# Kernel tuning notes

Hardware: AMD Instinct MI355X
Metric: run time of the kernel (lower is better)

## Reference

```python
import jax, jax.numpy as jnp
import numpy as np

K = 3   # kernel_size
D = 1   # dilation
G = 8   # groups
BN_EPS = 1e-5


def setup_inputs() -> dict:
    key = jax.random.key(0)
    ks = jax.random.split(key, 8)
    N, C, H, W = 8, 64, 256, 256
    k2 = K * K
    x = jax.random.normal(ks[0], (N, C, H, W), jnp.float32)
    conv_w = jax.random.normal(ks[1], (G * k2, C), jnp.float32) * (2.0 / C) ** 0.5
    bn_gamma = jnp.ones((G * k2,), jnp.float32)
    bn_beta = jnp.zeros((G * k2,), jnp.float32)
    bn_mean = jax.random.normal(ks[2], (G * k2,), jnp.float32) * 0.01
    bn_var = jax.random.uniform(ks[3], (G * k2,), jnp.float32, 0.5, 1.5)
    lamb_l = jax.random.normal(ks[4], (C,), jnp.float32) * 0.1
    lamb_h = jax.random.normal(ks[5], (C,), jnp.float32) * 0.1
    inside_all = jax.random.normal(ks[6], (C, 1, 1), jnp.float32) * 0.1
    return {"x": x, "conv_w": conv_w, "bn_gamma": bn_gamma, "bn_beta": bn_beta,
            "bn_mean": bn_mean, "bn_var": bn_var, "lamb_l": lamb_l,
            "lamb_h": lamb_h, "inside_all": inside_all}


def reference(x, conv_w, bn_gamma, bn_beta, bn_mean, bn_var, lamb_l, lamb_h, inside_all):
    N, C, H, W = x.shape
    k2 = K * K
    # ap: adaptive avg pool to (1,1) -> (N, C)
    pooled = x.mean(axis=(2, 3))
    # 1x1 conv on a 1x1 map == matmul; then eval-mode BatchNorm
    lf = pooled @ conv_w.T                                   # (N, G*k2)
    lf = (lf - bn_mean) * (bn_gamma / jnp.sqrt(bn_var + BN_EPS)) + bn_beta
    lf = jnp.tanh(lf).reshape(N, G, 1, k2, 1)                # (N, G, 1, k2, 1)
    # im2col/unfold with reflection padding; ordering matches torch (C, kh, kw)
    p = D * (K - 1) // 2
    xp = jnp.pad(x, ((0, 0), (0, 0), (p, p), (p, p)), mode="reflect")
    patches = jnp.stack(
        [xp[:, :, i * D:i * D + H, j * D:j * D + W] for i in range(K) for j in range(K)],
        axis=2,
    )                                                        # (N, C, k2, H, W)
    xu = patches.reshape(N, G, C // G, k2, H * W)
    low_part = jnp.sum(xu * lf, axis=3).reshape(N, C, H, W)  # per-pixel dynamic filter
    # DSA: gap pools to (1,1)
    gap = x.mean(axis=(2, 3), keepdims=True)                 # (N, C, 1, 1)
    out_low = (low_part * (inside_all + 1.0) - inside_all * gap) * lamb_l[None, :, None, None]
    out_high = x * (lamb_h[None, :, None, None] + 1.0)
    return out_low + out_high
```

## Files before the change

### kernel.cpp

```cpp
#include <hip/hip_runtime.h>
#include <math.h>

#define NN 8
#define CC 64
#define HH 256
#define WW 256
#define K2 9
#define OC 72
#define BN_EPS 1e-5f

typedef float f4 __attribute__((ext_vector_type(4)));

__global__ __launch_bounds__(1024) void pool_kernel(const float* __restrict__ x,
                                                    float* __restrict__ pooled) {
    int nc = blockIdx.x;
    const f4* p4 = (const f4*)(x + (size_t)nc * (HH * WW));
    float s = 0.f;
#pragma unroll 4
    for (int i = threadIdx.x; i < (HH * WW) / 4; i += 1024) {
        f4 v = p4[i];
        s += (v.x + v.y) + (v.z + v.w);
    }
    for (int off = 32; off > 0; off >>= 1) s += __shfl_down(s, off, 64);
    __shared__ float smem[16];
    int lane = threadIdx.x & 63, wid = threadIdx.x >> 6;
    if (lane == 0) smem[wid] = s;
    __syncthreads();
    if (threadIdx.x < 16) {
        float t = smem[threadIdx.x];
        for (int off = 8; off > 0; off >>= 1) t += __shfl_down(t, off, 64);
        if (threadIdx.x == 0) pooled[nc] = t * (1.0f / (HH * WW));
    }
}

__global__ __launch_bounds__(256, 3) void main_kernel(const float* __restrict__ x,
                                                      const float* __restrict__ conv_w,
                                                      const float* __restrict__ gamma,
                                                      const float* __restrict__ beta,
                                                      const float* __restrict__ mean,
                                                      const float* __restrict__ var,
                                                      const float* __restrict__ lamb_l,
                                                      const float* __restrict__ lamb_h,
                                                      const float* __restrict__ ia,
                                                      const float* __restrict__ pooled,
                                                      float* __restrict__ out) {
    const int bid  = (int)(blockIdx.x & 7) * 256 + (int)(blockIdx.x >> 3);
    const int wid  = threadIdx.x >> 6;
    const int lane = threadIdx.x & 63;
    const int nc   = bid >> 2;
    const int rb   = (bid & 3) << 6;
    const int r0a  = rb + (wid << 3);
    const int r0b  = rb + 32 + (wid << 3);
    const int c    = nc & (CC - 1);
    const int n    = nc >> 6;
    const int g    = c >> 3;

    const float* base    = x   + (size_t)nc * (HH * WW);
    float*       outbase = out + (size_t)nc * (HH * WW);

    f4 va[10], vb[10];
#pragma unroll
    for (int i = 0; i < 10; ++i) {
        int r = r0a - 1 + i;
        r = (r < 0) ? 1 : ((r > HH - 1) ? HH - 2 : r);
        va[i] = ((const f4*)(base + (size_t)r * WW))[lane];
    }
#pragma unroll
    for (int i = 0; i < 10; ++i) {
        int r = r0b - 1 + i;
        r = (r < 0) ? 1 : ((r > HH - 1) ? HH - 2 : r);
        vb[i] = ((const f4*)(base + (size_t)r * WW))[lane];
    }

    __shared__ float pl[CC];
    __shared__ float lfs[K2];
    if (threadIdx.x < CC) pl[threadIdx.x] = pooled[n * CC + threadIdx.x];
    __syncthreads();
    if (threadIdx.x < K2) {
        int oc = g * K2 + threadIdx.x;
        const float* pw = conv_w + oc * CC;
        float acc = 0.f;
#pragma unroll
        for (int cc2 = 0; cc2 < CC; ++cc2) acc += pl[cc2] * pw[cc2];
        float inv = gamma[oc] / sqrtf(var[oc] + BN_EPS);
        lfs[threadIdx.x] = tanhf((acc - mean[oc]) * inv + beta[oc]);
    }
    __syncthreads();

    const float w00 = lfs[0], w01 = lfs[1], w02 = lfs[2];
    const float w10 = lfs[3], w11 = lfs[4], w12 = lfs[5];
    const float w20 = lfs[6], w21 = lfs[7], w22 = lfs[8];
    const float ll    = lamb_l[c];
    const float lh1   = lamb_h[c] + 1.0f;
    const float iav   = ia[c];
    const float scale = iav + 1.0f;
    const float bias  = -iav * pl[c];

#define CONV_CHUNK(V, R0)                                                        \
    {                                                                            \
        float L[10], R[10];                                                      \
        _Pragma("unroll")                                                        \
        for (int i = 0; i < 10; ++i) {                                           \
            L[i] = __shfl_up(V[i].w, 1, 64);   if (lane == 0)  L[i] = V[i].y;    \
            R[i] = __shfl_down(V[i].x, 1, 64); if (lane == 63) R[i] = V[i].z;    \
        }                                                                        \
        _Pragma("unroll")                                                        \
        for (int j = 0; j < 8; ++j) {                                            \
            const float t[6]  = {L[j],   V[j].x,   V[j].y,   V[j].z,   V[j].w,   R[j]};   \
            const float m[6]  = {L[j+1], V[j+1].x, V[j+1].y, V[j+1].z, V[j+1].w, R[j+1]}; \
            const float bb[6] = {L[j+2], V[j+2].x, V[j+2].y, V[j+2].z, V[j+2].w, R[j+2]}; \
            f4 o;                                                                \
            _Pragma("unroll")                                                    \
            for (int k = 0; k < 4; ++k) {                                        \
                float acc = w00 * t[k]  + w01 * t[k + 1]  + w02 * t[k + 2]       \
                          + w10 * m[k]  + w11 * m[k + 1]  + w12 * m[k + 2]       \
                          + w20 * bb[k] + w21 * bb[k + 1] + w22 * bb[k + 2];     \
                o[k] = ll * (scale * acc + bias) + lh1 * m[k + 1];               \
            }                                                                    \
            __builtin_nontemporal_store(o, ((f4*)(outbase + (size_t)((R0) + j) * WW)) + lane); \
        }                                                                        \
    }

    CONV_CHUNK(va, r0a)
    CONV_CHUNK(vb, r0b)
#undef CONV_CHUNK
}

extern "C" void kernel_launch(void* const* d_in, const int* in_sizes, int n_in,
                              void* d_out, int out_size, void* d_ws, size_t ws_size,
                              hipStream_t stream) {
    const float* x      = (const float*)d_in[0];
    const float* conv_w = (const float*)d_in[1];
    const float* gamma  = (const float*)d_in[2];
    const float* beta   = (const float*)d_in[3];
    const float* mean   = (const float*)d_in[4];
    const float* var    = (const float*)d_in[5];
    const float* lamb_l = (const float*)d_in[6];
    const float* lamb_h = (const float*)d_in[7];
    const float* ia     = (const float*)d_in[8];
    float* out = (float*)d_out;

    float* pooled = (float*)d_ws;

    pool_kernel<<<NN * CC, 1024, 0, stream>>>(x, pooled);
    main_kernel<<<NN * CC * (HH / 64), 256, 0, stream>>>(x, conv_w, gamma, beta,
                                                         mean, var, lamb_l, lamb_h,
                                                         ia, pooled, out);
}
```

Baseline: 264.7 us.

## Fuse pooling into main kernel with inter-block ready flags

Merges the separate pooling kernel into the main kernel. Each of 1024 blocks sums half a channel plane, publishes its partial sum with a release-store flag, then spin-waits until all 128 partials for its batch image are ready. It then computes the dynamic filter and processes 128 rows in four chunks. This removes one kernel launch and lets the second read of x hit in cache. The price is a memset, a reliance on all blocks being co-resident for the spin-wait to finish, and fewer, larger blocks.

```diff
diff --git a/kernel.cpp b/kernel.cpp
--- a/kernel.cpp
+++ b/kernel.cpp
@@ -8,73 +8,83 @@
 #define K2 9
 #define OC 72
 #define BN_EPS 1e-5f
+#define NBLK 1024
 
 typedef float f4 __attribute__((ext_vector_type(4)));
 
-__global__ __launch_bounds__(1024) void pool_kernel(const float* __restrict__ x,
-                                                    float* __restrict__ pooled) {
-    int nc = blockIdx.x;
-    const f4* p4 = (const f4*)(x + (size_t)nc * (HH * WW));
-    float s = 0.f;
-#pragma unroll 4
-    for (int i = threadIdx.x; i < (HH * WW) / 4; i += 1024) {
-        f4 v = p4[i];
-        s += (v.x + v.y) + (v.z + v.w);
-    }
-    for (int off = 32; off > 0; off >>= 1) s += __shfl_down(s, off, 64);
-    __shared__ float smem[16];
-    int lane = threadIdx.x & 63, wid = threadIdx.x >> 6;
-    if (lane == 0) smem[wid] = s;
-    __syncthreads();
-    if (threadIdx.x < 16) {
-        float t = smem[threadIdx.x];
-        for (int off = 8; off > 0; off >>= 1) t += __shfl_down(t, off, 64);
-        if (threadIdx.x == 0) pooled[nc] = t * (1.0f / (HH * WW));
-    }
-}
-
-__global__ __launch_bounds__(256, 3) void main_kernel(const float* __restrict__ x,
-                                                      const float* __restrict__ conv_w,
-                                                      const float* __restrict__ gamma,
-                                                      const float* __restrict__ beta,
-                                                      const float* __restrict__ mean,
-                                                      const float* __restrict__ var,
-                                                      const float* __restrict__ lamb_l,
-                                                      const float* __restrict__ lamb_h,
-                                                      const float* __restrict__ ia,
-                                                      const float* __restrict__ pooled,
-                                                      float* __restrict__ out) {
-    const int bid  = (int)(blockIdx.x & 7) * 256 + (int)(blockIdx.x >> 3);
+__global__ __launch_bounds__(256, 4) void fused_kernel(
+    const float* __restrict__ x,
+    const float* __restrict__ conv_w,
+    const float* __restrict__ gamma,
+    const float* __restrict__ beta,
+    const float* __restrict__ mean,
+    const float* __restrict__ var,
+    const float* __restrict__ lamb_l,
+    const float* __restrict__ lamb_h,
+    const float* __restrict__ ia,
+    float* __restrict__ out,
+    float* __restrict__ ws)
+{
+    const int bid  = (int)(blockIdx.x & 7) * 128 + (int)(blockIdx.x >> 3);
     const int wid  = threadIdx.x >> 6;
     const int lane = threadIdx.x & 63;
-    const int nc   = bid >> 2;
-    const int rb   = (bid & 3) << 6;
-    const int r0a  = rb + (wid << 3);
-    const int r0b  = rb + 32 + (wid << 3);
+    const int nc   = bid >> 1;
+    const int half = bid & 1;
     const int c    = nc & (CC - 1);
     const int n    = nc >> 6;
     const int g    = c >> 3;
 
     const float* base    = x   + (size_t)nc * (HH * WW);
     float*       outbase = out + (size_t)nc * (HH * WW);
+    int*         ready   = (int*)(ws + NBLK);
 
-    f4 va[10], vb[10];
-#pragma unroll
-    for (int i = 0; i < 10; ++i) {
-        int r = r0a - 1 + i;
-        r = (r < 0) ? 1 : ((r > HH - 1) ? HH - 2 : r);
-        va[i] = ((const f4*)(base + (size_t)r * WW))[lane];
+    float s = 0.f;
+    {
+        const int rbase = half * 128 + wid * 32;
+#pragma unroll 8
+        for (int i = 0; i < 32; ++i) {
+            f4 v = ((const f4*)(base + (size_t)(rbase + i) * WW))[lane];
+            s += (v.x + v.y) + (v.z + v.w);
+        }
     }
-#pragma unroll
-    for (int i = 0; i < 10; ++i) {
-        int r = r0b - 1 + i;
-        r = (r < 0) ? 1 : ((r > HH - 1) ? HH - 2 : r);
-        vb[i] = ((const f4*)(base + (size_t)r * WW))[lane];
+    for (int off = 32; off > 0; off >>= 1) s += __shfl_down(s, off, 64);
+    __shared__ float red[4];
+    if (lane == 0) red[wid] = s;
+    __syncthreads();
+    if (threadIdx.x == 0) {
+        float t = (red[0] + red[1]) + (red[2] + red[3]);
+        ws[bid] = t;
+        __hip_atomic_store(&ready[bid], 1, __ATOMIC_RELEASE,
+                           __HIP_MEMORY_SCOPE_AGENT);
     }
 
+    f4 v0[10];
+    {
+        const int r0 = half * 128 + wid * 8;
+#pragma unroll
+        for (int i = 0; i < 10; ++i) {
+            int r = r0 - 1 + i;
+            r = (r < 0) ? 1 : ((r > HH - 1) ? HH - 2 : r);
+            v0[i] = ((const f4*)(base + (size_t)r * WW))[lane];
+        }
+    }
+
+    if (threadIdx.x < 128) {
+        while (__hip_atomic_load(&ready[n * 128 + threadIdx.x], __ATOMIC_ACQUIRE,
+                                 __HIP_MEMORY_SCOPE_AGENT) == 0) {
+            __builtin_amdgcn_s_sleep(2);
+        }
+    }
+    __syncthreads();
+
+    __shared__ float part[128];
     __shared__ float pl[CC];
     __shared__ float lfs[K2];
-    if (threadIdx.x < CC) pl[threadIdx.x] = pooled[n * CC + threadIdx.x];
+    if (threadIdx.x < 128) part[threadIdx.x] = ws[n * 128 + threadIdx.x];
+    __syncthreads();
+    if (threadIdx.x < CC)
+        pl[threadIdx.x] = (part[2 * threadIdx.x] + part[2 * threadIdx.x + 1])
+                          * (1.0f / (HH * WW));
     __syncthreads();
     if (threadIdx.x < K2) {
         int oc = g * K2 + threadIdx.x;
@@ -121,8 +131,19 @@
         }                                                                        \
     }
 
-    CONV_CHUNK(va, r0a)
-    CONV_CHUNK(vb, r0b)
+    CONV_CHUNK(v0, half * 128 + wid * 8)
+
+    for (int chunk = 1; chunk < 4; ++chunk) {
+        const int r0 = half * 128 + chunk * 32 + wid * 8;
+        f4 v[10];
+#pragma unroll
+        for (int i = 0; i < 10; ++i) {
+            int r = r0 - 1 + i;
+            r = (r < 0) ? 1 : ((r > HH - 1) ? HH - 2 : r);
+            v[i] = ((const f4*)(base + (size_t)r * WW))[lane];
+        }
+        CONV_CHUNK(v, r0)
+    }
 #undef CONV_CHUNK
 }
 
@@ -139,11 +160,9 @@
     const float* lamb_h = (const float*)d_in[7];
     const float* ia     = (const float*)d_in[8];
     float* out = (float*)d_out;
+    float* ws  = (float*)d_ws;
 
-    float* pooled = (float*)d_ws;
-
-    pool_kernel<<<NN * CC, 1024, 0, stream>>>(x, pooled);
-    main_kernel<<<NN * CC * (HH / 64), 256, 0, stream>>>(x, conv_w, gamma, beta,
-                                                         mean, var, lamb_l, lamb_h,
-                                                         ia, pooled, out);
+    hipMemsetAsync(ws, 0, 2 * NBLK * sizeof(float), stream);
+    fused_kernel<<<NBLK, 256, 0, stream>>>(x, conv_w, gamma, beta, mean, var,
+                                           lamb_l, lamb_h, ia, out, ws);
 }
```

Result: slower. 362.7 us (+37.0%).
